# Performance work log

Measured on AMD Instinct MI355X. Metric: run time of the kernel, lower is better.

## Reference

```python
import jax, jax.numpy as jnp
import numpy as np

DIM, D_STATE, D_CONV, EXPAND = 384, 16, 4, 2
D_INNER = EXPAND * DIM          # 768
DT_RANK = -(-DIM // 16)         # 24
B_, T_, H_, W_ = 2, 8, 16, 16
EPS = 1e-5


def layernorm(x, w, b):
    mu = x.mean(-1, keepdims=True)
    var = ((x - mu) ** 2).mean(-1, keepdims=True)
    return (x - mu) * jax.lax.rsqrt(var + EPS) * w + b


def setup_inputs() -> dict:
    key = jax.random.key(0)
    ks = jax.random.split(key, 12)
    std = 0.02
    x = jax.random.normal(ks[0], (B_, DIM, T_, H_, W_), jnp.float32)
    params = dict(
        ln1_w=jnp.ones((DIM,), jnp.float32),
        ln1_b=jnp.zeros((DIM,), jnp.float32),
        ln2_w=jnp.ones((DIM,), jnp.float32),
        ln2_b=jnp.zeros((DIM,), jnp.float32),
        in_proj_w=std * jax.random.normal(ks[1], (2 * D_INNER, DIM), jnp.float32),
        conv_w=std * jax.random.normal(ks[2], (D_INNER, 1, D_CONV), jnp.float32),
        conv_b=jnp.zeros((D_INNER,), jnp.float32),
        x_proj_w=std * jax.random.normal(ks[3], (DT_RANK + 2 * D_STATE, D_INNER), jnp.float32),
        dt_proj_w=std * jax.random.normal(ks[4], (D_INNER, DT_RANK), jnp.float32),
        dt_proj_b=0.01 * jax.random.normal(ks[5], (D_INNER,), jnp.float32),
        A_log=jnp.log(jnp.broadcast_to(jnp.arange(1, D_STATE + 1, dtype=jnp.float32), (D_INNER, D_STATE))),
        D=jnp.ones((D_INNER,), jnp.float32),
        out_proj_w=std * jax.random.normal(ks[6], (DIM, D_INNER), jnp.float32),
    )
    return {"x": x, **params}


def mamba(xn, in_proj_w, conv_w, conv_b, x_proj_w, dt_proj_w, dt_proj_b, A_log, D, out_proj_w):
    # xn: [B, L, dim]
    B, L, _ = xn.shape
    xz = xn @ in_proj_w.T                      # [B, L, 2*d_inner]
    u, z = jnp.split(xz, 2, axis=-1)
    # causal depthwise conv over tokens
    uc = jnp.transpose(u, (0, 2, 1))           # [B, d_inner, L]
    uc = jax.lax.conv_general_dilated(
        uc, conv_w, window_strides=(1,), padding=[(D_CONV - 1, 0)],
        dimension_numbers=("NCH", "OIH", "NCH"), feature_group_count=D_INNER)
    u = jax.nn.silu(jnp.transpose(uc, (0, 2, 1)) + conv_b)  # [B, L, d_inner]

    dbc = u @ x_proj_w.T                       # [B, L, dt_rank + 2*d_state]
    dt = dbc[..., :DT_RANK]
    Bm = dbc[..., DT_RANK:DT_RANK + D_STATE]   # [B, L, d_state]
    Cm = dbc[..., DT_RANK + D_STATE:]          # [B, L, d_state]
    delta = jax.nn.softplus(dt @ dt_proj_w.T + dt_proj_b)   # [B, L, d_inner]

    A = -jnp.exp(A_log)                        # [d_inner, d_state]
    deltaA = jnp.exp(delta[..., None] * A)                     # [B, L, d_inner, d_state]
    deltaBu = delta[..., None] * Bm[:, :, None, :] * u[..., None]

    def step(h, inp):
        dA, dBu, c = inp                       # [B,d_inner,d_state], [B,d_inner,d_state], [B,d_state]
        h = dA * h + dBu
        y = jnp.einsum("bds,bs->bd", h, c)
        return h, y

    h0 = jnp.zeros((B, D_INNER, D_STATE), xn.dtype)
    xs = (jnp.moveaxis(deltaA, 1, 0), jnp.moveaxis(deltaBu, 1, 0), jnp.moveaxis(Cm, 1, 0))
    _, ys = jax.lax.scan(step, h0, xs)
    y = jnp.moveaxis(ys, 0, 1)                 # [B, L, d_inner]
    y = y + u * D
    y = y * jax.nn.silu(z)
    return y @ out_proj_w.T                    # [B, L, dim]


def reference(x, ln1_w, ln1_b, ln2_w, ln2_b, in_proj_w, conv_w, conv_b,
              x_proj_w, dt_proj_w, dt_proj_b, A_log, D, out_proj_w):
    B, C, T, H, W = x.shape
    L = T * H * W
    x_flat = jnp.transpose(x.reshape(B, C, L), (0, 2, 1))   # [B, L, C]
    x_norm = layernorm(x_flat, ln1_w, ln1_b)
    x_mamba = mamba(x_norm, in_proj_w, conv_w, conv_b, x_proj_w,
                    dt_proj_w, dt_proj_b, A_log, D, out_proj_w)
    x_out = layernorm(x_flat + x_mamba, ln2_w, ln2_b)
    return jnp.transpose(x_out, (0, 2, 1)).reshape(B, C, T, H, W)
```

## Files before the change

kernel.cpp:

```cpp
#include <hip/hip_runtime.h>
#include <hip/hip_bf16.h>

typedef unsigned short u16;
typedef unsigned int   u32;
typedef __attribute__((ext_vector_type(8))) short short8;
typedef __attribute__((ext_vector_type(4))) float f32x4;

#define B_   2
#define L_   2048
#define CDIM 384
#define DI   768
#define DXZ  1536
#define DTR  24
#define DS   16
#define NDBC 56
#define NC   64
#define TC   32
#define TL   32
#define EPSV 1e-5f

#define OFFW_WIN  0
#define OFFW_WXP  589824
#define OFFW_WOUT 632832
#define TOTW      927744

__device__ __forceinline__ float bf2f(u16 u) {
    union { u32 i; float f; } v; v.i = ((u32)u) << 16; return v.f;
}
__device__ __forceinline__ u16 f2bf(float f) {
    union { float f; u32 i; } v; v.f = f;
    u32 x = v.i;
    u32 r = (x + 0x7FFFu + ((x >> 16) & 1u)) >> 16;
    return (u16)r;
}

__global__ __launch_bounds__(256) void ln1_convert(const float* __restrict__ x,
                                                   const float* __restrict__ w,
                                                   const float* __restrict__ bb,
                                                   u16* __restrict__ xn,
                                                   const float* __restrict__ win,
                                                   const float* __restrict__ wxp,
                                                   const float* __restrict__ wout,
                                                   u16* __restrict__ wdst) {
    __shared__ float tile[CDIM][TL + 1];
    __shared__ float red_s[8][TL];
    __shared__ float red_s2[8][TL];
    __shared__ float mu_s[TL], rs_s[TL];
    int tid = threadIdx.x, blk = blockIdx.x;
    if (blk >= 128) {
        int base = (blk - 128) * 256 + tid;
        for (int e = base; e < TOTW; e += 128 * 256) {
            float v;
            if (e < OFFW_WXP)       v = win[e];
            else if (e < OFFW_WOUT) v = wxp[e - OFFW_WXP];
            else                    v = wout[e - OFFW_WOUT];
            wdst[e] = f2bf(v);
        }
        return;
    }
    int b = blk >> 6;
    int l0 = (blk & 63) * TL;
    int cg = tid >> 5, li = tid & 31;
    const float* xp = x + (size_t)b * CDIM * L_ + l0 + li;
    float s = 0.f, s2 = 0.f;
#pragma unroll
    for (int c = cg; c < CDIM; c += 8) {
        float v = xp[(size_t)c * L_];
        tile[c][li] = v;
        s += v; s2 += v * v;
    }
    red_s[cg][li] = s; red_s2[cg][li] = s2;
    __syncthreads();
    if (tid < TL) {
        float ts = 0.f, ts2 = 0.f;
#pragma unroll
        for (int g = 0; g < 8; g++) { ts += red_s[g][tid]; ts2 += red_s2[g][tid]; }
        float mu = ts / CDIM;
        float var = ts2 / CDIM - mu * mu;
        mu_s[tid] = mu; rs_s[tid] = rsqrtf(var + EPSV);
    }
    __syncthreads();
    int wv = tid >> 6, lane = tid & 63;
#pragma unroll
    for (int r = 0; r < 8; r++) {
        int l = wv * 8 + r;
        float mu = mu_s[l], rs = rs_s[l];
        u16* op = xn + (size_t)(b * L_ + l0 + l) * CDIM;
#pragma unroll
        for (int j = 0; j < 6; j++) {
            int c = lane + 64 * j;
            float t = (tile[c][l] - mu) * rs * w[c] + bb[c];
            op[c] = f2bf(t);
        }
    }
}

template<int KN>
__global__ __launch_bounds__(256) void gemm_in(const u16* __restrict__ A,
                                               const u16* __restrict__ Bm,
                                               u16* __restrict__ Cp, int Nn) {
    int wave = threadIdx.x >> 6, lane = threadIdx.x & 63;
    int wm = wave & 1, wn = wave >> 1;
    int m0 = (blockIdx.x * 2 + wm) * 64;
    int n0 = (blockIdx.y * 2 + wn) * 64;
    int r = lane & 15, q = lane >> 4;
    f32x4 acc[4][4];
#pragma unroll
    for (int i = 0; i < 4; i++)
#pragma unroll
        for (int j = 0; j < 4; j++)
#pragma unroll
            for (int g = 0; g < 4; g++) acc[i][j][g] = 0.f;
#pragma unroll
    for (int k0 = 0; k0 < KN; k0 += 32) {
        short8 af[4], bf[4];
        int ka = k0 + q * 8;
#pragma unroll
        for (int i = 0; i < 4; i++) {
            af[i] = *(const short8*)(A + (size_t)(m0 + i * 16 + r) * KN + ka);
            bf[i] = *(const short8*)(Bm + (size_t)(n0 + i * 16 + r) * KN + ka);
        }
#pragma unroll
        for (int i = 0; i < 4; i++)
#pragma unroll
            for (int j = 0; j < 4; j++)
                acc[i][j] = __builtin_amdgcn_mfma_f32_16x16x32_bf16(af[i], bf[j], acc[i][j], 0, 0, 0);
    }
#pragma unroll
    for (int i = 0; i < 4; i++)
#pragma unroll
        for (int j = 0; j < 4; j++) {
            int col = n0 + j * 16 + r;
#pragma unroll
            for (int g = 0; g < 4; g++)
                Cp[(size_t)(m0 + i * 16 + q * 4 + g) * Nn + col] = f2bf(acc[i][j][g]);
        }
}

template<int KN, int NN>
__global__ __launch_bounds__(64) void gemm_out(const u16* __restrict__ A,
                                               const u16* __restrict__ Bm,
                                               float* __restrict__ Cp) {
    int lane = threadIdx.x;
    int m0 = blockIdx.x * 64, n0 = blockIdx.y * 64;
    int r = lane & 15, q = lane >> 4;
    f32x4 acc[4][4];
#pragma unroll
    for (int i = 0; i < 4; i++)
#pragma unroll
        for (int j = 0; j < 4; j++)
#pragma unroll
            for (int g = 0; g < 4; g++) acc[i][j][g] = 0.f;
#pragma unroll
    for (int k0 = 0; k0 < KN; k0 += 32) {
        short8 af[4], bf[4];
        int ka = k0 + q * 8;
#pragma unroll
        for (int i = 0; i < 4; i++) {
            af[i] = *(const short8*)(A + (size_t)(m0 + i * 16 + r) * KN + ka);
            bf[i] = *(const short8*)(Bm + (size_t)(n0 + i * 16 + r) * KN + ka);
        }
#pragma unroll
        for (int i = 0; i < 4; i++)
#pragma unroll
            for (int j = 0; j < 4; j++)
                acc[i][j] = __builtin_amdgcn_mfma_f32_16x16x32_bf16(af[i], bf[j], acc[i][j], 0, 0, 0);
    }
#pragma unroll
    for (int i = 0; i < 4; i++)
#pragma unroll
        for (int j = 0; j < 4; j++) {
            int col = n0 + j * 16 + r;
#pragma unroll
            for (int g = 0; g < 4; g++)
                Cp[(size_t)(m0 + i * 16 + q * 4 + g) * NN + col] = acc[i][j][g];
        }
}

template<int KN>
__global__ __launch_bounds__(64) void gemm_xp(const u16* __restrict__ A,
                                              const u16* __restrict__ Bm,
                                              float* __restrict__ Cp) {
    int lane = threadIdx.x;
    int m0 = blockIdx.x * 16;
    int r = lane & 15, q = lane >> 4;
    f32x4 acc[4];
#pragma unroll
    for (int j = 0; j < 4; j++)
#pragma unroll
        for (int g = 0; g < 4; g++) acc[j][g] = 0.f;
    short8 zf;
#pragma unroll
    for (int e = 0; e < 8; e++) zf[e] = 0;
#pragma unroll
    for (int k0 = 0; k0 < KN; k0 += 32) {
        int ka = k0 + q * 8;
        short8 af = *(const short8*)(A + (size_t)(m0 + r) * KN + ka);
        short8 bf[4];
#pragma unroll
        for (int j = 0; j < 4; j++) {
            int n = j * 16 + r;
            bf[j] = (n < NDBC) ? *(const short8*)(Bm + (size_t)n * KN + ka) : zf;
        }
#pragma unroll
        for (int j = 0; j < 4; j++)
            acc[j] = __builtin_amdgcn_mfma_f32_16x16x32_bf16(af, bf[j], acc[j], 0, 0, 0);
    }
#pragma unroll
    for (int j = 0; j < 4; j++) {
        int col = j * 16 + r;
        if (col < NDBC) {
#pragma unroll
            for (int g = 0; g < 4; g++)
                Cp[(size_t)(m0 + q * 4 + g) * NDBC + col] = acc[j][g];
        }
    }
}

__global__ __launch_bounds__(256) void conv_silu(const u16* __restrict__ xz,
                                                 const float* __restrict__ cw,
                                                 const float* __restrict__ cb,
                                                 u16* __restrict__ ubf) {
    int d = blockIdx.y * 256 + threadIdx.x;
    int m0 = blockIdx.x * 16;
    int l0 = m0 & (L_ - 1);
    float4 c4 = ((const float4*)cw)[d];
    float bias = cb[d];
    float w0, w1, w2;
    if (l0 == 0) { w0 = w1 = w2 = 0.f; }
    else {
        w0 = bf2f(xz[(size_t)(m0 - 3) * DXZ + d]);
        w1 = bf2f(xz[(size_t)(m0 - 2) * DXZ + d]);
        w2 = bf2f(xz[(size_t)(m0 - 1) * DXZ + d]);
    }
#pragma unroll
    for (int i = 0; i < 16; i++) {
        int m = m0 + i;
        float cur = bf2f(xz[(size_t)m * DXZ + d]);
        float acc = bias + w0 * c4.x + w1 * c4.y + w2 * c4.z + cur * c4.w;
        float sg = 1.f / (1.f + __expf(-acc));
        ubf[(size_t)m * DI + d] = f2bf(acc * sg);
        w0 = w1; w1 = w2; w2 = cur;
    }
}

__global__ __launch_bounds__(256) void scan_pass1(const u16* __restrict__ ubf,
                                                  const float* __restrict__ dbc,
                                                  const float* __restrict__ alogf,
                                                  const float* __restrict__ wdtf,
                                                  const float* __restrict__ bdtf,
                                                  float* __restrict__ chA,
                                                  float* __restrict__ chB) {
    int bc = blockIdx.x;
    int b = bc >> 6, chunk = bc & 63;
    int d = blockIdx.y * 256 + threadIdx.x;
    float a[DS], ap[DS], bv[DS], wdt[DTR];
#pragma unroll
    for (int s = 0; s < DS; s++) { a[s] = -__expf(alogf[d * DS + s]); ap[s] = 1.f; bv[s] = 0.f; }
#pragma unroll
    for (int k = 0; k < DTR; k++) wdt[k] = wdtf[d * DTR + k];
    float bd = bdtf[d];
    int t0 = b * L_ + chunk * TC;
#pragma unroll 2
    for (int t = t0; t < t0 + TC; t++) {
        const float* row = dbc + (size_t)t * NDBC;
        float acc = bd;
#pragma unroll
        for (int k = 0; k < DTR; k++) acc += row[k] * wdt[k];
        float dd = (acc > 20.f) ? acc : __logf(1.f + __expf(acc));
        float du = dd * bf2f(ubf[(size_t)t * DI + d]);
#pragma unroll
        for (int s = 0; s < DS; s++) {
            float dA = __expf(dd * a[s]);
            bv[s] = dA * bv[s] + du * row[DTR + s];
            ap[s] *= dA;
        }
    }
    float* pa = chA + ((size_t)bc * DI + d) * DS;
    float* pb = chB + ((size_t)bc * DI + d) * DS;
#pragma unroll
    for (int s = 0; s < DS; s++) { pa[s] = ap[s]; pb[s] = bv[s]; }
}

__global__ __launch_bounds__(256) void scan_mid(const float* __restrict__ chA,
                                                const float* __restrict__ chB,
                                                float* __restrict__ hin) {
    int idx = blockIdx.x * 256 + threadIdx.x;
    int b = idx / (DI * DS);
    int rem = idx - b * (DI * DS);
    float h = 0.f;
#pragma unroll 4
    for (int c = 0; c < NC; c++) {
        size_t off = ((size_t)(b * NC + c) * DI) * DS + rem;
        hin[off] = h;
        h = chA[off] * h + chB[off];
    }
}

__global__ __launch_bounds__(256) void scan_pass2(const u16* __restrict__ ubf,
                                                  const float* __restrict__ dbc,
                                                  const float* __restrict__ alogf,
                                                  const float* __restrict__ wdtf,
                                                  const float* __restrict__ bdtf,
                                                  const float* __restrict__ hin,
                                                  const float* __restrict__ Dwf,
                                                  const u16* __restrict__ xz,
                                                  u16* __restrict__ ym) {
    int bc = blockIdx.x;
    int b = bc >> 6, chunk = bc & 63;
    int d = blockIdx.y * 256 + threadIdx.x;
    float a[DS], h[DS], wdt[DTR];
#pragma unroll
    for (int s = 0; s < DS; s++) a[s] = -__expf(alogf[d * DS + s]);
#pragma unroll
    for (int k = 0; k < DTR; k++) wdt[k] = wdtf[d * DTR + k];
    float bd = bdtf[d];
    const float* hp = hin + ((size_t)bc * DI + d) * DS;
    float h0[DS];
#pragma unroll
    for (int s = 0; s < DS; s++) h[s] = hp[s];
    float dD = Dwf[d];
    int t0 = b * L_ + chunk * TC;
#pragma unroll 2
    for (int t = t0; t < t0 + TC; t++) {
        const float* row = dbc + (size_t)t * NDBC;
        float acc = bd;
#pragma unroll
        for (int k = 0; k < DTR; k++) acc += row[k] * wdt[k];
        float dd = (acc > 20.f) ? acc : __logf(1.f + __expf(acc));
        float uu = bf2f(ubf[(size_t)t * DI + d]);
        float du = dd * uu;
        float y = 0.f;
#pragma unroll
        for (int s = 0; s < DS; s++) {
            float dA = __expf(dd * a[s]);
            h[s] = dA * h[s] + du * row[DTR + s];
            y += h[s] * row[DTR + DS + s];
        }
        float z = bf2f(xz[(size_t)t * DXZ + DI + d]);
        float sg = 1.f / (1.f + __expf(-z));
        ym[(size_t)t * DI + d] = f2bf((y + uu * dD) * (z * sg));
    }
}

__global__ __launch_bounds__(256) void ln2_out(const float* __restrict__ x,
                                               const float* __restrict__ om,
                                               const float* __restrict__ w,
                                               const float* __restrict__ bb,
                                               float* __restrict__ out) {
    __shared__ float tile[CDIM][TL + 1];
    __shared__ float mu_s[TL], rs_s[TL];
    int tid = threadIdx.x, blk = blockIdx.x;
    int b = blk >> 6;
    int l0 = (blk & 63) * TL;
    int cg = tid >> 5, li = tid & 31;
    const float* xp = x + (size_t)b * CDIM * L_ + l0 + li;
#pragma unroll
    for (int c = cg; c < CDIM; c += 8) tile[c][li] = xp[(size_t)c * L_];
    __syncthreads();
    int wv = tid >> 6, lane = tid & 63;
#pragma unroll
    for (int r = 0; r < 8; r++) {
        int l = wv * 8 + r;
        const float* op = om + (size_t)(b * L_ + l0 + l) * CDIM;
        float s = 0.f, s2 = 0.f;
#pragma unroll
        for (int j = 0; j < 6; j++) {
            int c = lane + 64 * j;
            float t = tile[c][l] + op[c];
            tile[c][l] = t;
            s += t; s2 += t * t;
        }
#pragma unroll
        for (int off = 32; off > 0; off >>= 1) { s += __shfl_xor(s, off); s2 += __shfl_xor(s2, off); }
        if (lane == 0) {
            float mu = s / CDIM;
            float var = s2 / CDIM - mu * mu;
            mu_s[l] = mu; rs_s[l] = rsqrtf(var + EPSV);
        }
    }
    __syncthreads();
    float* outp = out + (size_t)b * CDIM * L_ + l0 + li;
    float mu = mu_s[li], rs = rs_s[li];
#pragma unroll
    for (int c = cg; c < CDIM; c += 8) {
        float t = (tile[c][li] - mu) * rs * w[c] + bb[c];
        outp[(size_t)c * L_] = t;
    }
}

extern "C" void kernel_launch(void* const* d_in, const int* in_sizes, int n_in,
                              void* d_out, int out_size, void* d_ws, size_t ws_size,
                              hipStream_t stream) {
    const float* x    = (const float*)d_in[0];
    const float* ln1w = (const float*)d_in[1];
    const float* ln1b = (const float*)d_in[2];
    const float* ln2w = (const float*)d_in[3];
    const float* ln2b = (const float*)d_in[4];
    const float* win  = (const float*)d_in[5];
    const float* cw   = (const float*)d_in[6];
    const float* cb   = (const float*)d_in[7];
    const float* wxp  = (const float*)d_in[8];
    const float* wdt  = (const float*)d_in[9];
    const float* bdt  = (const float*)d_in[10];
    const float* alog = (const float*)d_in[11];
    const float* Dw   = (const float*)d_in[12];
    const float* wout = (const float*)d_in[13];

    char* ws = (char*)d_ws;
    u16*   wbf   = (u16*)(ws + 0);
    u16*   win_b  = wbf + OFFW_WIN;
    u16*   wxp_b  = wbf + OFFW_WXP;
    u16*   wout_b = wbf + OFFW_WOUT;
    u16*   xn    = (u16*)(ws + 1855488);
    u16*   xz    = (u16*)(ws + 5001216);
    u16*   ubf   = (u16*)(ws + 17584128);
    float* dbc   = (float*)(ws + 23875584);
    float* chA   = (float*)(ws + 24793088);
    float* chB   = (float*)(ws + 31084544);
    float* hin   = (float*)(ws + 37376000);
    u16*   ym    = (u16*)(ws + 43667456);
    float* om    = (float*)(ws + 49958912);

    ln1_convert<<<dim3(256), 256, 0, stream>>>(x, ln1w, ln1b, xn, win, wxp, wout, wbf);
    gemm_in<384><<<dim3(32, 12), 256, 0, stream>>>(xn, win_b, xz, DXZ);
    conv_silu<<<dim3(256, 3), 256, 0, stream>>>(xz, cw, cb, ubf);
    gemm_xp<768><<<dim3(256), 64, 0, stream>>>(ubf, wxp_b, dbc);
    scan_pass1<<<dim3(128, 3), 256, 0, stream>>>(ubf, dbc, alog, wdt, bdt, chA, chB);
    scan_mid<<<96, 256, 0, stream>>>(chA, chB, hin);
    scan_pass2<<<dim3(128, 3), 256, 0, stream>>>(ubf, dbc, alog, wdt, bdt, hin, Dw, xz, ym);
    gemm_out<768, 384><<<dim3(64, 6), 64, 0, stream>>>(ym, wout_b, om);
    ln2_out<<<dim3(128), 256, 0, stream>>>(x, om, ln2w, ln2b, (float*)d_out);
}
```

Baseline: 223.4 us.

## Fuse causal conv+SiLU with x_proj GEMM using shared-memory u tile

Merges the depthwise causal conv/SiLU kernel and the x_proj GEMM into one kernel. Each block computes 32 rows of u into LDS, writes them to global for the scan, then runs MFMA on the LDS tile to produce dbc. This removes one launch and the global re-read of u by the GEMM. The cost is fewer blocks (128 instead of 768 and 256), less parallelism in the conv phase, and a serialized conv-then-GEMM inside each block.

After: 235.1 us. 1.05x slower.

```diff
diff --git a/kernel.cpp b/kernel.cpp
--- a/kernel.cpp
+++ b/kernel.cpp
@@ -177,70 +177,67 @@
         }
 }
 
-template<int KN>
-__global__ __launch_bounds__(64) void gemm_xp(const u16* __restrict__ A,
-                                              const u16* __restrict__ Bm,
-                                              float* __restrict__ Cp) {
-    int lane = threadIdx.x;
-    int m0 = blockIdx.x * 16;
+__global__ __launch_bounds__(256) void conv_xp(const u16* __restrict__ xz,
+                                               const float* __restrict__ cw,
+                                               const float* __restrict__ cb,
+                                               const u16* __restrict__ wxpb,
+                                               u16* __restrict__ ubf,
+                                               float* __restrict__ dbc) {
+    __shared__ u16 u_s[32][DI + 8];
+    int tid = threadIdx.x;
+    int m0 = blockIdx.x * 32;
+    int l0 = m0 & (L_ - 1);
+#pragma unroll
+    for (int dd = 0; dd < 3; dd++) {
+        int d = tid + dd * 256;
+        float4 c4 = ((const float4*)cw)[d];
+        float bias = cb[d];
+        float w0, w1, w2;
+        if (l0 == 0) { w0 = w1 = w2 = 0.f; }
+        else {
+            w0 = bf2f(xz[(size_t)(m0 - 3) * DXZ + d]);
+            w1 = bf2f(xz[(size_t)(m0 - 2) * DXZ + d]);
+            w2 = bf2f(xz[(size_t)(m0 - 1) * DXZ + d]);
+        }
+#pragma unroll
+        for (int i = 0; i < 32; i++) {
+            int m = m0 + i;
+            float cur = bf2f(xz[(size_t)m * DXZ + d]);
+            float acc = bias + w0 * c4.x + w1 * c4.y + w2 * c4.z + cur * c4.w;
+            float sg = 1.f / (1.f + __expf(-acc));
+            u16 uv = f2bf(acc * sg);
+            u_s[i][d] = uv;
+            ubf[(size_t)m * DI + d] = uv;
+            w0 = w1; w1 = w2; w2 = cur;
+        }
+    }
+    __syncthreads();
+    int wave = tid >> 6, lane = tid & 63;
     int r = lane & 15, q = lane >> 4;
-    f32x4 acc[4];
-#pragma unroll
-    for (int j = 0; j < 4; j++)
-#pragma unroll
-        for (int g = 0; g < 4; g++) acc[j][g] = 0.f;
+    int mt = (wave >> 1) * 16;
+    int nt = (wave & 1) * 32;
+    f32x4 acc0, acc1;
+#pragma unroll
+    for (int g = 0; g < 4; g++) { acc0[g] = 0.f; acc1[g] = 0.f; }
     short8 zf;
 #pragma unroll
     for (int e = 0; e < 8; e++) zf[e] = 0;
 #pragma unroll
-    for (int k0 = 0; k0 < KN; k0 += 32) {
+    for (int k0 = 0; k0 < DI; k0 += 32) {
         int ka = k0 + q * 8;
-        short8 af = *(const short8*)(A + (size_t)(m0 + r) * KN + ka);
-        short8 bf[4];
-#pragma unroll
-        for (int j = 0; j < 4; j++) {
-            int n = j * 16 + r;
-            bf[j] = (n < NDBC) ? *(const short8*)(Bm + (size_t)n * KN + ka) : zf;
-        }
-#pragma unroll
-        for (int j = 0; j < 4; j++)
-            acc[j] = __builtin_amdgcn_mfma_f32_16x16x32_bf16(af, bf[j], acc[j], 0, 0, 0);
-    }
-#pragma unroll
-    for (int j = 0; j < 4; j++) {
-        int col = j * 16 + r;
-        if (col < NDBC) {
-#pragma unroll
-            for (int g = 0; g < 4; g++)
-                Cp[(size_t)(m0 + q * 4 + g) * NDBC + col] = acc[j][g];
-        }
-    }
-}
-
-__global__ __launch_bounds__(256) void conv_silu(const u16* __restrict__ xz,
-                                                 const float* __restrict__ cw,
-                                                 const float* __restrict__ cb,
-                                                 u16* __restrict__ ubf) {
-    int d = blockIdx.y * 256 + threadIdx.x;
-    int m0 = blockIdx.x * 16;
-    int l0 = m0 & (L_ - 1);
-    float4 c4 = ((const float4*)cw)[d];
-    float bias = cb[d];
-    float w0, w1, w2;
-    if (l0 == 0) { w0 = w1 = w2 = 0.f; }
-    else {
-        w0 = bf2f(xz[(size_t)(m0 - 3) * DXZ + d]);
-        w1 = bf2f(xz[(size_t)(m0 - 2) * DXZ + d]);
-        w2 = bf2f(xz[(size_t)(m0 - 1) * DXZ + d]);
-    }
-#pragma unroll
-    for (int i = 0; i < 16; i++) {
-        int m = m0 + i;
-        float cur = bf2f(xz[(size_t)m * DXZ + d]);
-        float acc = bias + w0 * c4.x + w1 * c4.y + w2 * c4.z + cur * c4.w;
-        float sg = 1.f / (1.f + __expf(-acc));
-        ubf[(size_t)m * DI + d] = f2bf(acc * sg);
-        w0 = w1; w1 = w2; w2 = cur;
+        short8 af = *(const short8*)(&u_s[mt + r][ka]);
+        int n0 = nt + r, n1 = nt + 16 + r;
+        short8 b0 = (n0 < NDBC) ? *(const short8*)(wxpb + (size_t)n0 * DI + ka) : zf;
+        short8 b1 = (n1 < NDBC) ? *(const short8*)(wxpb + (size_t)n1 * DI + ka) : zf;
+        acc0 = __builtin_amdgcn_mfma_f32_16x16x32_bf16(af, b0, acc0, 0, 0, 0);
+        acc1 = __builtin_amdgcn_mfma_f32_16x16x32_bf16(af, b1, acc1, 0, 0, 0);
+    }
+#pragma unroll
+    for (int g = 0; g < 4; g++) {
+        int row = m0 + mt + q * 4 + g;
+        int c0 = nt + r, c1 = nt + 16 + r;
+        if (c0 < NDBC) dbc[(size_t)row * NDBC + c0] = acc0[g];
+        if (c1 < NDBC) dbc[(size_t)row * NDBC + c1] = acc1[g];
     }
 }
 
@@ -316,7 +313,6 @@
     for (int k = 0; k < DTR; k++) wdt[k] = wdtf[d * DTR + k];
     float bd = bdtf[d];
     const float* hp = hin + ((size_t)bc * DI + d) * DS;
-    float h0[DS];
 #pragma unroll
     for (int s = 0; s < DS; s++) h[s] = hp[s];
     float dD = Dwf[d];
@@ -424,8 +420,7 @@
 
     ln1_convert<<<dim3(256), 256, 0, stream>>>(x, ln1w, ln1b, xn, win, wxp, wout, wbf);
     gemm_in<384><<<dim3(32, 12), 256, 0, stream>>>(xn, win_b, xz, DXZ);
-    conv_silu<<<dim3(256, 3), 256, 0, stream>>>(xz, cw, cb, ubf);
-    gemm_xp<768><<<dim3(256), 64, 0, stream>>>(ubf, wxp_b, dbc);
+    conv_xp<<<dim3(128), 256, 0, stream>>>(xz, cw, cb, wxp_b, ubf, dbc);
     scan_pass1<<<dim3(128, 3), 256, 0, stream>>>(ubf, dbc, alog, wdt, bdt, chA, chB);
     scan_mid<<<96, 256, 0, stream>>>(chA, chB, hin);
     scan_pass2<<<dim3(128, 3), 256, 0, stream>>>(ubf, dbc, alog, wdt, bdt, hin, Dw, xz, ym);
```

## Fuse out-projection GEMM with residual add and LayerNorm2 in one kernel

Applied to the files above, without the earlier changes.

Replaces the separate out_proj GEMM and ln2 kernel with one kernel. Each 256-thread block computes a 64-row by 384-column output tile with MFMA, stages it as bf16 in shared memory, then adds the residual, computes LayerNorm statistics and writes the transposed output. This removes the fp32 intermediate round trip through global memory and one launch. In exchange only 64 blocks run, which lowers parallelism, and the GEMM result is rounded to bf16 before the residual add.

After: 264.5 us. 18.4% more time.

```diff
diff --git a/kernel.cpp b/kernel.cpp
--- a/kernel.cpp
+++ b/kernel.cpp
@@ -137,86 +137,6 @@
         }
 }
 
-template<int KN, int NN>
-__global__ __launch_bounds__(64) void gemm_out(const u16* __restrict__ A,
-                                               const u16* __restrict__ Bm,
-                                               float* __restrict__ Cp) {
-    int lane = threadIdx.x;
-    int m0 = blockIdx.x * 64, n0 = blockIdx.y * 64;
-    int r = lane & 15, q = lane >> 4;
-    f32x4 acc[4][4];
-#pragma unroll
-    for (int i = 0; i < 4; i++)
-#pragma unroll
-        for (int j = 0; j < 4; j++)
-#pragma unroll
-            for (int g = 0; g < 4; g++) acc[i][j][g] = 0.f;
-#pragma unroll
-    for (int k0 = 0; k0 < KN; k0 += 32) {
-        short8 af[4], bf[4];
-        int ka = k0 + q * 8;
-#pragma unroll
-        for (int i = 0; i < 4; i++) {
-            af[i] = *(const short8*)(A + (size_t)(m0 + i * 16 + r) * KN + ka);
-            bf[i] = *(const short8*)(Bm + (size_t)(n0 + i * 16 + r) * KN + ka);
-        }
-#pragma unroll
-        for (int i = 0; i < 4; i++)
-#pragma unroll
-            for (int j = 0; j < 4; j++)
-                acc[i][j] = __builtin_amdgcn_mfma_f32_16x16x32_bf16(af[i], bf[j], acc[i][j], 0, 0, 0);
-    }
-#pragma unroll
-    for (int i = 0; i < 4; i++)
-#pragma unroll
-        for (int j = 0; j < 4; j++) {
-            int col = n0 + j * 16 + r;
-#pragma unroll
-            for (int g = 0; g < 4; g++)
-                Cp[(size_t)(m0 + i * 16 + q * 4 + g) * NN + col] = acc[i][j][g];
-        }
-}
-
-template<int KN>
-__global__ __launch_bounds__(64) void gemm_xp(const u16* __restrict__ A,
-                                              const u16* __restrict__ Bm,
-                                              float* __restrict__ Cp) {
-    int lane = threadIdx.x;
-    int m0 = blockIdx.x * 16;
-    int r = lane & 15, q = lane >> 4;
-    f32x4 acc[4];
-#pragma unroll
-    for (int j = 0; j < 4; j++)
-#pragma unroll
-        for (int g = 0; g < 4; g++) acc[j][g] = 0.f;
-    short8 zf;
-#pragma unroll
-    for (int e = 0; e < 8; e++) zf[e] = 0;
-#pragma unroll
-    for (int k0 = 0; k0 < KN; k0 += 32) {
-        int ka = k0 + q * 8;
-        short8 af = *(const short8*)(A + (size_t)(m0 + r) * KN + ka);
-        short8 bf[4];
-#pragma unroll
-        for (int j = 0; j < 4; j++) {
-            int n = j * 16 + r;
-            bf[j] = (n < NDBC) ? *(const short8*)(Bm + (size_t)n * KN + ka) : zf;
-        }
-#pragma unroll
-        for (int j = 0; j < 4; j++)
-            acc[j] = __builtin_amdgcn_mfma_f32_16x16x32_bf16(af, bf[j], acc[j], 0, 0, 0);
-    }
-#pragma unroll
-    for (int j = 0; j < 4; j++) {
-        int col = j * 16 + r;
-        if (col < NDBC) {
-#pragma unroll
-            for (int g = 0; g < 4; g++)
-                Cp[(size_t)(m0 + q * 4 + g) * NDBC + col] = acc[j][g];
-        }
-    }
-}
-
 __global__ __launch_bounds__(256) void conv_silu(const u16* __restrict__ xz,
                                                  const float* __restrict__ cw,
                                                  const float* __restrict__ cb,
@@ -244,6 +164,46 @@
     }
 }
 
+template<int KN>
+__global__ __launch_bounds__(64) void gemm_xp(const u16* __restrict__ A,
+                                              const u16* __restrict__ Bm,
+                                              float* __restrict__ Cp) {
+    int lane = threadIdx.x;
+    int m0 = blockIdx.x * 16;
+    int r = lane & 15, q = lane >> 4;
+    f32x4 acc[4];
+#pragma unroll
+    for (int j = 0; j < 4; j++)
+#pragma unroll
+        for (int g = 0; g < 4; g++) acc[j][g] = 0.f;
+    short8 zf;
+#pragma unroll
+    for (int e = 0; e < 8; e++) zf[e] = 0;
+#pragma unroll
+    for (int k0 = 0; k0 < KN; k0 += 32) {
+        int ka = k0 + q * 8;
+        short8 af = *(const short8*)(A + (size_t)(m0 + r) * KN + ka);
+        short8 bf[4];
+#pragma unroll
+        for (int j = 0; j < 4; j++) {
+            int n = j * 16 + r;
+            bf[j] = (n < NDBC) ? *(const short8*)(Bm + (size_t)n * KN + ka) : zf;
+        }
+#pragma unroll
+        for (int j = 0; j < 4; j++)
+            acc[j] = __builtin_amdgcn_mfma_f32_16x16x32_bf16(af, bf[j], acc[j], 0, 0, 0);
+    }
+#pragma unroll
+    for (int j = 0; j < 4; j++) {
+        int col = j * 16 + r;
+        if (col < NDBC) {
+#pragma unroll
+            for (int g = 0; g < 4; g++)
+                Cp[(size_t)(m0 + q * 4 + g) * NDBC + col] = acc[j][g];
+        }
+    }
+}
+
 __global__ __launch_bounds__(256) void scan_pass1(const u16* __restrict__ ubf,
                                                   const float* __restrict__ dbc,
                                                   const float* __restrict__ alogf,
@@ -316,7 +276,6 @@
     for (int k = 0; k < DTR; k++) wdt[k] = wdtf[d * DTR + k];
     float bd = bdtf[d];
     const float* hp = hin + ((size_t)bc * DI + d) * DS;
-    float h0[DS];
 #pragma unroll
     for (int s = 0; s < DS; s++) h[s] = hp[s];
     float dD = Dwf[d];
@@ -343,49 +302,79 @@
     }
 }
 
-__global__ __launch_bounds__(256) void ln2_out(const float* __restrict__ x,
-                                               const float* __restrict__ om,
+#define CS_STRIDE 390
+__global__ __launch_bounds__(256) void out_ln2(const u16* __restrict__ ym,
+                                               const u16* __restrict__ woutb,
+                                               const float* __restrict__ x,
                                                const float* __restrict__ w,
                                                const float* __restrict__ bb,
                                                float* __restrict__ out) {
-    __shared__ float tile[CDIM][TL + 1];
-    __shared__ float mu_s[TL], rs_s[TL];
-    int tid = threadIdx.x, blk = blockIdx.x;
-    int b = blk >> 6;
-    int l0 = (blk & 63) * TL;
-    int cg = tid >> 5, li = tid & 31;
-    const float* xp = x + (size_t)b * CDIM * L_ + l0 + li;
-#pragma unroll
-    for (int c = cg; c < CDIM; c += 8) tile[c][li] = xp[(size_t)c * L_];
+    __shared__ u16 cs[64 * CS_STRIDE];
+    __shared__ float ps[4][64], ps2[4][64];
+    __shared__ float mu_s[64], rs_s[64];
+    int tid = threadIdx.x;
+    int wave = tid >> 6, lane = tid & 63;
+    int r = lane & 15, q = lane >> 4;
+    int m0 = blockIdx.x * 64;
+    f32x4 acc[4][6];
+#pragma unroll
+    for (int i = 0; i < 4; i++)
+#pragma unroll
+        for (int j = 0; j < 6; j++)
+#pragma unroll
+            for (int g = 0; g < 4; g++) acc[i][j][g] = 0.f;
+#pragma unroll 2
+    for (int k0 = 0; k0 < DI; k0 += 32) {
+        int ka = k0 + q * 8;
+        short8 af[4], bf[6];
+#pragma unroll
+        for (int i = 0; i < 4; i++)
+            af[i] = *(const short8*)(ym + (size_t)(m0 + i * 16 + r) * DI + ka);
+#pragma unroll
+        for (int j = 0; j < 6; j++)
+            bf[j] = *(const short8*)(woutb + (size_t)(wave * 96 + j * 16 + r) * DI + ka);
+#pragma unroll
+        for (int i = 0; i < 4; i++)
+#pragma unroll
+            for (int j = 0; j < 6; j++)
+                acc[i][j] = __builtin_amdgcn_mfma_f32_16x16x32_bf16(af[i], bf[j], acc[i][j], 0, 0, 0);
+    }
+#pragma unroll
+    for (int i = 0; i < 4; i++)
+#pragma unroll
+        for (int j = 0; j < 6; j++) {
+            int col = wave * 96 + j * 16 + r;
+#pragma unroll
+            for (int g = 0; g < 4; g++)
+                cs[(i * 16 + q * 4 + g) * CS_STRIDE + col] = f2bf(acc[i][j][g]);
+        }
     __syncthreads();
-    int wv = tid >> 6, lane = tid & 63;
-#pragma unroll
-    for (int r = 0; r < 8; r++) {
-        int l = wv * 8 + r;
-        const float* op = om + (size_t)(b * L_ + l0 + l) * CDIM;
-        float s = 0.f, s2 = 0.f;
-#pragma unroll
-        for (int j = 0; j < 6; j++) {
-            int c = lane + 64 * j;
-            float t = tile[c][l] + op[c];
-            tile[c][l] = t;
-            s += t; s2 += t * t;
-        }
-#pragma unroll
-        for (int off = 32; off > 0; off >>= 1) { s += __shfl_xor(s, off); s2 += __shfl_xor(s2, off); }
-        if (lane == 0) {
-            float mu = s / CDIM;
-            float var = s2 / CDIM - mu * mu;
-            mu_s[l] = mu; rs_s[l] = rsqrtf(var + EPSV);
-        }
-    }
+    int li = tid & 63, cgr = tid >> 6;
+    int rowg = m0 + li;
+    int b = rowg >> 11, l = rowg & (L_ - 1);
+    const float* xcol = x + (size_t)b * CDIM * L_ + l;
+    float s = 0.f, s2 = 0.f;
+#pragma unroll
+    for (int c = cgr; c < CDIM; c += 4) {
+        float t = bf2f(cs[li * CS_STRIDE + c]) + xcol[(size_t)c * L_];
+        s += t; s2 += t * t;
+    }
+    ps[cgr][li] = s; ps2[cgr][li] = s2;
     __syncthreads();
-    float* outp = out + (size_t)b * CDIM * L_ + l0 + li;
+    if (tid < 64) {
+        float ts = ps[0][tid] + ps[1][tid] + ps[2][tid] + ps[3][tid];
+        float ts2 = ps2[0][tid] + ps2[1][tid] + ps2[2][tid] + ps2[3][tid];
+        float mu = ts / CDIM;
+        float var = ts2 / CDIM - mu * mu;
+        mu_s[tid] = mu; rs_s[tid] = rsqrtf(var + EPSV);
+    }
+    __syncthreads();
     float mu = mu_s[li], rs = rs_s[li];
-#pragma unroll
-    for (int c = cg; c < CDIM; c += 8) {
-        float t = (tile[c][li] - mu) * rs * w[c] + bb[c];
-        outp[(size_t)c * L_] = t;
+    float* op = out + (size_t)b * CDIM * L_ + l;
+#pragma unroll
+    for (int c = cgr; c < CDIM; c += 4) {
+        float t = bf2f(cs[li * CS_STRIDE + c]) + xcol[(size_t)c * L_];
+        op[(size_t)c * L_] = (t - mu) * rs * w[c] + bb[c];
     }
 }
 
@@ -420,7 +409,6 @@
     float* chB   = (float*)(ws + 31084544);
     float* hin   = (float*)(ws + 37376000);
     u16*   ym    = (u16*)(ws + 43667456);
-    float* om    = (float*)(ws + 49958912);
 
     ln1_convert<<<dim3(256), 256, 0, stream>>>(x, ln1w, ln1b, xn, win, wxp, wout, wbf);
     gemm_in<384><<<dim3(32, 12), 256, 0, stream>>>(xn, win_b, xz, DXZ);
@@ -429,6 +417,5 @@
     scan_pass1<<<dim3(128, 3), 256, 0, stream>>>(ubf, dbc, alog, wdt, bdt, chA, chB);
     scan_mid<<<96, 256, 0, stream>>>(chA, chB, hin);
     scan_pass2<<<dim3(128, 3), 256, 0, stream>>>(ubf, dbc, alog, wdt, bdt, hin, Dw, xz, ym);
-    gemm_out<768, 384><<<dim3(64, 6), 64, 0, stream>>>(ym, wout_b, om);
-    ln2_out<<<dim3(128), 256, 0, stream>>>(x, om, ln2w, ln2b, (float*)d_out);
-}
+    out_ln2<<<dim3(64), 256, 0, stream>>>(ym, wout_b, x, ln2w, ln2b, (float*)d_out);
+}
```

## Fold chunk-prefix scan into pass2 and split GEMM tiles across four waves

Applied to the files above, without the earlier changes.

Removes the scan_mid kernel. Each scan_pass2 thread now recomputes its incoming state by walking the chunk summaries of all earlier chunks, which removes one launch and the hin round trip at the cost of redundant work that grows with the chunk index. The gemm_xp and gemm_out kernels are rewritten so each 256-thread block spreads the N or M tile across four waves instead of one wave doing all of it. This raises the number of active waves and lowers register pressure per wave, but each wave reloads the shared operand.

Measured after the change: 280.9 us. 25.8% more time.

```diff
diff --git a/kernel.cpp b/kernel.cpp
--- a/kernel.cpp
+++ b/kernel.cpp
@@ -137,86 +137,6 @@
         }
 }
 
-template<int KN, int NN>
-__global__ __launch_bounds__(64) void gemm_out(const u16* __restrict__ A,
-                                               const u16* __restrict__ Bm,
-                                               float* __restrict__ Cp) {
-    int lane = threadIdx.x;
-    int m0 = blockIdx.x * 64, n0 = blockIdx.y * 64;
-    int r = lane & 15, q = lane >> 4;
-    f32x4 acc[4][4];
-#pragma unroll
-    for (int i = 0; i < 4; i++)
-#pragma unroll
-        for (int j = 0; j < 4; j++)
-#pragma unroll
-            for (int g = 0; g < 4; g++) acc[i][j][g] = 0.f;
-#pragma unroll
-    for (int k0 = 0; k0 < KN; k0 += 32) {
-        short8 af[4], bf[4];
-        int ka = k0 + q * 8;
-#pragma unroll
-        for (int i = 0; i < 4; i++) {
-            af[i] = *(const short8*)(A + (size_t)(m0 + i * 16 + r) * KN + ka);
-            bf[i] = *(const short8*)(Bm + (size_t)(n0 + i * 16 + r) * KN + ka);
-        }
-#pragma unroll
-        for (int i = 0; i < 4; i++)
-#pragma unroll
-            for (int j = 0; j < 4; j++)
-                acc[i][j] = __builtin_amdgcn_mfma_f32_16x16x32_bf16(af[i], bf[j], acc[i][j], 0, 0, 0);
-    }
-#pragma unroll
-    for (int i = 0; i < 4; i++)
-#pragma unroll
-        for (int j = 0; j < 4; j++) {
-            int col = n0 + j * 16 + r;
-#pragma unroll
-            for (int g = 0; g < 4; g++)
-                Cp[(size_t)(m0 + i * 16 + q * 4 + g) * NN + col] = acc[i][j][g];
-        }
-}
-
-template<int KN>
-__global__ __launch_bounds__(64) void gemm_xp(const u16* __restrict__ A,
-                                              const u16* __restrict__ Bm,
-                                              float* __restrict__ Cp) {
-    int lane = threadIdx.x;
-    int m0 = blockIdx.x * 16;
-    int r = lane & 15, q = lane >> 4;
-    f32x4 acc[4];
-#pragma unroll
-    for (int j = 0; j < 4; j++)
-#pragma unroll
-        for (int g = 0; g < 4; g++) acc[j][g] = 0.f;
-    short8 zf;
-#pragma unroll
-    for (int e = 0; e < 8; e++) zf[e] = 0;
-#pragma unroll
-    for (int k0 = 0; k0 < KN; k0 += 32) {
-        int ka = k0 + q * 8;
-        short8 af = *(const short8*)(A + (size_t)(m0 + r) * KN + ka);
-        short8 bf[4];
-#pragma unroll
-        for (int j = 0; j < 4; j++) {
-            int n = j * 16 + r;
-            bf[j] = (n < NDBC) ? *(const short8*)(Bm + (size_t)n * KN + ka) : zf;
-        }
-#pragma unroll
-        for (int j = 0; j < 4; j++)
-            acc[j] = __builtin_amdgcn_mfma_f32_16x16x32_bf16(af, bf[j], acc[j], 0, 0, 0);
-    }
-#pragma unroll
-    for (int j = 0; j < 4; j++) {
-        int col = j * 16 + r;
-        if (col < NDBC) {
-#pragma unroll
-            for (int g = 0; g < 4; g++)
-                Cp[(size_t)(m0 + q * 4 + g) * NDBC + col] = acc[j][g];
-        }
-    }
-}
-
 __global__ __launch_bounds__(256) void conv_silu(const u16* __restrict__ xz,
                                                  const float* __restrict__ cw,
                                                  const float* __restrict__ cb,
@@ -244,6 +164,34 @@
     }
 }
 
+__global__ __launch_bounds__(256) void gemm_xp(const u16* __restrict__ A,
+                                               const u16* __restrict__ Bm,
+                                               float* __restrict__ Cp) {
+    int tid = threadIdx.x;
+    int wave = tid >> 6, lane = tid & 63;
+    int m0 = blockIdx.x * 16;
+    int r = lane & 15, q = lane >> 4;
+    int nr = wave * 16 + r;
+    f32x4 acc;
+#pragma unroll
+    for (int g = 0; g < 4; g++) acc[g] = 0.f;
+    short8 zf;
+#pragma unroll
+    for (int e = 0; e < 8; e++) zf[e] = 0;
+#pragma unroll
+    for (int k0 = 0; k0 < DI; k0 += 32) {
+        int ka = k0 + q * 8;
+        short8 af = *(const short8*)(A + (size_t)(m0 + r) * DI + ka);
+        short8 bf = (nr < NDBC) ? *(const short8*)(Bm + (size_t)nr * DI + ka) : zf;
+        acc = __builtin_amdgcn_mfma_f32_16x16x32_bf16(af, bf, acc, 0, 0, 0);
+    }
+    if (nr < NDBC) {
+#pragma unroll
+        for (int g = 0; g < 4; g++)
+            Cp[(size_t)(m0 + q * 4 + g) * NDBC + nr] = acc[g];
+    }
+}
+
 __global__ __launch_bounds__(256) void scan_pass1(const u16* __restrict__ ubf,
                                                   const float* __restrict__ dbc,
                                                   const float* __restrict__ alogf,
@@ -282,27 +230,13 @@
     for (int s = 0; s < DS; s++) { pa[s] = ap[s]; pb[s] = bv[s]; }
 }
 
-__global__ __launch_bounds__(256) void scan_mid(const float* __restrict__ chA,
-                                                const float* __restrict__ chB,
-                                                float* __restrict__ hin) {
-    int idx = blockIdx.x * 256 + threadIdx.x;
-    int b = idx / (DI * DS);
-    int rem = idx - b * (DI * DS);
-    float h = 0.f;
-#pragma unroll 4
-    for (int c = 0; c < NC; c++) {
-        size_t off = ((size_t)(b * NC + c) * DI) * DS + rem;
-        hin[off] = h;
-        h = chA[off] * h + chB[off];
-    }
-}
-
 __global__ __launch_bounds__(256) void scan_pass2(const u16* __restrict__ ubf,
                                                   const float* __restrict__ dbc,
                                                   const float* __restrict__ alogf,
                                                   const float* __restrict__ wdtf,
                                                   const float* __restrict__ bdtf,
-                                                  const float* __restrict__ hin,
+                                                  const float* __restrict__ chA,
+                                                  const float* __restrict__ chB,
                                                   const float* __restrict__ Dwf,
                                                   const u16* __restrict__ xz,
                                                   u16* __restrict__ ym) {
@@ -311,14 +245,16 @@
     int d = blockIdx.y * 256 + threadIdx.x;
     float a[DS], h[DS], wdt[DTR];
 #pragma unroll
-    for (int s = 0; s < DS; s++) a[s] = -__expf(alogf[d * DS + s]);
+    for (int s = 0; s < DS; s++) { a[s] = -__expf(alogf[d * DS + s]); h[s] = 0.f; }
+    for (int c = 0; c < chunk; c++) {
+        const float* pa = chA + ((size_t)(b * NC + c) * DI + d) * DS;
+        const float* pb = chB + ((size_t)(b * NC + c) * DI + d) * DS;
+#pragma unroll
+        for (int s = 0; s < DS; s++) h[s] = pa[s] * h[s] + pb[s];
+    }
 #pragma unroll
     for (int k = 0; k < DTR; k++) wdt[k] = wdtf[d * DTR + k];
     float bd = bdtf[d];
-    const float* hp = hin + ((size_t)bc * DI + d) * DS;
-    float h0[DS];
-#pragma unroll
-    for (int s = 0; s < DS; s++) h[s] = hp[s];
     float dD = Dwf[d];
     int t0 = b * L_ + chunk * TC;
 #pragma unroll 2
@@ -340,6 +276,38 @@
         float z = bf2f(xz[(size_t)t * DXZ + DI + d]);
         float sg = 1.f / (1.f + __expf(-z));
         ym[(size_t)t * DI + d] = f2bf((y + uu * dD) * (z * sg));
+    }
+}
+
+__global__ __launch_bounds__(256) void gemm_out(const u16* __restrict__ A,
+                                                const u16* __restrict__ Bm,
+                                                float* __restrict__ Cp) {
+    int tid = threadIdx.x;
+    int wave = tid >> 6, lane = tid & 63;
+    int r = lane & 15, q = lane >> 4;
+    int m0 = blockIdx.x * 64 + wave * 16;
+    int n0 = blockIdx.y * 64;
+    f32x4 acc[4];
+#pragma unroll
+    for (int j = 0; j < 4; j++)
+#pragma unroll
+        for (int g = 0; g < 4; g++) acc[j][g] = 0.f;
+#pragma unroll 4
+    for (int k0 = 0; k0 < DI; k0 += 32) {
+        int ka = k0 + q * 8;
+        short8 af = *(const short8*)(A + (size_t)(m0 + r) * DI + ka);
+#pragma unroll
+        for (int j = 0; j < 4; j++) {
+            short8 bf = *(const short8*)(Bm + (size_t)(n0 + j * 16 + r) * DI + ka);
+            acc[j] = __builtin_amdgcn_mfma_f32_16x16x32_bf16(af, bf, acc[j], 0, 0, 0);
+        }
+    }
+#pragma unroll
+    for (int j = 0; j < 4; j++) {
+        int col = n0 + j * 16 + r;
+#pragma unroll
+        for (int g = 0; g < 4; g++)
+            Cp[(size_t)(m0 + q * 4 + g) * CDIM + col] = acc[j][g];
     }
 }
 
@@ -418,17 +386,15 @@
     float* dbc   = (float*)(ws + 23875584);
     float* chA   = (float*)(ws + 24793088);
     float* chB   = (float*)(ws + 31084544);
-    float* hin   = (float*)(ws + 37376000);
     u16*   ym    = (u16*)(ws + 43667456);
     float* om    = (float*)(ws + 49958912);
 
     ln1_convert<<<dim3(256), 256, 0, stream>>>(x, ln1w, ln1b, xn, win, wxp, wout, wbf);
     gemm_in<384><<<dim3(32, 12), 256, 0, stream>>>(xn, win_b, xz, DXZ);
     conv_silu<<<dim3(256, 3), 256, 0, stream>>>(xz, cw, cb, ubf);
-    gemm_xp<768><<<dim3(256), 64, 0, stream>>>(ubf, wxp_b, dbc);
+    gemm_xp<<<dim3(256), 256, 0, stream>>>(ubf, wxp_b, dbc);
     scan_pass1<<<dim3(128, 3), 256, 0, stream>>>(ubf, dbc, alog, wdt, bdt, chA, chB);
-    scan_mid<<<96, 256, 0, stream>>>(chA, chB, hin);
-    scan_pass2<<<dim3(128, 3), 256, 0, stream>>>(ubf, dbc, alog, wdt, bdt, hin, Dw, xz, ym);
-    gemm_out<768, 384><<<dim3(64, 6), 64, 0, stream>>>(ym, wout_b, om);
+    scan_pass2<<<dim3(128, 3), 256, 0, stream>>>(ubf, dbc, alog, wdt, bdt, chA, chB, Dw, xz, ym);
+    gemm_out<<<dim3(64, 6), 256, 0, stream>>>(ym, wout_b, om);
     ln2_out<<<dim3(128), 256, 0, stream>>>(x, om, ln2w, ln2b, (float*)d_out);
 }
```
